# Performance work log

Hardware: AMD Instinct MI355X
Metric: run time of the kernel (lower is better)

## Reference

```python
import jax, jax.numpy as jnp
import numpy as np

NEG_SLOPE = 0.2
EPS = 1e-6


def setup_inputs() -> dict:
    key = jax.random.key(0)
    k1, k2 = jax.random.split(key)
    B, C, N = 4, 64, 32768
    x = jax.random.normal(k1, (B, C, 3, N), dtype=jnp.float32)
    # VNLinear weight: nn.Linear(in, out, bias=False).weight -> [out, in]
    W = jax.random.normal(k2, (C, C), dtype=jnp.float32) * (1.0 / np.sqrt(C))
    return {"x": x, "W": W}


def reference(x, W):
    # VNLinear: kron(W, eye(3)) conv2d == per-3-vector channel mix
    # d[b,o,v,n] = sum_i W[o,i] * x[b,i,v,n]
    d = jnp.einsum('oi,bivn->bovn', W, x)
    dotprod = jnp.sum(x * d, axis=2, keepdims=True)      # [B,C,1,N]
    d_norm_sq = jnp.sum(d * d, axis=2, keepdims=True)    # [B,C,1,N]
    neg = x - (1.0 - NEG_SLOPE) * (dotprod / (d_norm_sq + EPS)) * d
    return jnp.where(dotprod >= 0, x, neg)
```

## Files before the change

kernel.cpp:

```cpp
#include <hip/hip_runtime.h>

#define NEG_SLOPE 0.2f
#define EPS 1e-6f


#define C_CH 64
#define V_DIM 3
#define N_FULL 32768
#define NT 32
#define THREADS 256
#define TPB 4

typedef __attribute__((ext_vector_type(8))) short bf16x8;
typedef __attribute__((ext_vector_type(4))) float f32x4;

__device__ __forceinline__ ushort f2bf(float f) {
    union { float f; unsigned u; } v; v.f = f;
    unsigned r = v.u + 0x7FFFu + ((v.u >> 16) & 1u);
    return (ushort)(r >> 16);
}
__device__ __forceinline__ float bf2f(ushort s) {
    union { unsigned u; float f; } v; v.u = ((unsigned)s) << 16; return v.f;
}
__device__ __forceinline__ unsigned f2u(float f) {
    union { float f; unsigned u; } v; v.f = f; return v.u;
}
__device__ __forceinline__ float u2f(unsigned u) {
    union { unsigned u; float f; } v; v.u = u; return v.f;
}

__global__ __launch_bounds__(THREADS, 3)
void vn_dma_pipe(const float* __restrict__ x,
                 const float* __restrict__ Wf,
                 float* __restrict__ out) {
    __shared__ float xs[2][V_DIM * C_CH * NT];

    const int t     = threadIdx.x;
    const int tile0 = blockIdx.x * TPB;
    const int b     = tile0 >> 10;
    const float* xbase = x   + (size_t)b * (C_CH * V_DIM * N_FULL);
    float*       obase = out + (size_t)b * (C_CH * V_DIM * N_FULL);

    const int lane = t & 63;
    const int w    = t >> 6;
    const int wo   = w >> 1;
    const int wn   = w & 1;
    const int l4   = lane & 15;
    const int hi   = lane >> 4;

    const int slot_r[6] = { (t + 0*THREADS) >> 3, (t + 1*THREADS) >> 3,
                            (t + 2*THREADS) >> 3, (t + 3*THREADS) >> 3,
                            (t + 4*THREADS) >> 3, (t + 5*THREADS) >> 3 };

    bf16x8 Ah[2][2], Al[2][2];
    #pragma unroll
    for (int m = 0; m < 2; ++m)
        #pragma unroll
        for (int kh = 0; kh < 2; ++kh) {
            const float* wp = Wf + (size_t)(wo * 32 + m * 16 + l4) * C_CH + kh * 32 + hi * 8;
            float4 wa = *(const float4*)wp;
            float4 wb = *(const float4*)(wp + 4);
            float wf[8] = {wa.x, wa.y, wa.z, wa.w, wb.x, wb.y, wb.z, wb.w};
            bf16x8 h, l;
            #pragma unroll
            for (int j = 0; j < 8; ++j) {
                ushort hb = f2bf(wf[j]);
                h[j] = (short)hb;
                l[j] = (short)f2bf(wf[j] - bf2f(hb));
            }
            Ah[m][kh] = h; Al[m][kh] = l;
        }

    bf16x8 Aid0, Aid1;
    {
        const int j1 = l4 & 7;
        const bool h0 = (hi == (l4 >> 3));
        const bool h1 = (hi == 2 + (l4 >> 3));
        #pragma unroll
        for (int j = 0; j < 8; ++j) {
            Aid0[j] = (short)((h0 && j == j1) ? 0x3F80 : 0);
            Aid1[j] = (short)((h1 && j == j1) ? 0x3F80 : 0);
        }
    }

    auto stage = [&](int tile, int bf) {
        const float* xb = xbase + ((tile & 1023) << 5);
        #pragma unroll
        for (int it = 0; it < 6; ++it) {
            int slot = t + it * THREADS;
            int r    = slot_r[it];
            int c    = slot & 7;
            int i    = (r * 171) >> 9;
            int cs   = c ^ (((i >> 3) & 1) << 2);
            const float* g = xb + (size_t)r * N_FULL + (cs << 2);
            void* l = (char*)&xs[bf][0] + (size_t)slot * 16;
            __builtin_amdgcn_global_load_lds(
                (const __attribute__((address_space(1))) unsigned*)g,
                (__attribute__((address_space(3))) unsigned*)l, 16, 0, 0);
        }
    };

    stage(tile0, 0);
    __syncthreads();

    const int acol = (wn * 16 + l4) ^ ((hi & 1) << 4);
    const int n    = wn * 16 + l4;

    #pragma unroll
    for (int tt = 0; tt < TPB; ++tt) {
        const int cur = tt & 1;
        const int n0c = ((tile0 + tt) & 1023) << 5;

        if (tt + 1 < TPB) stage(tile0 + tt + 1, cur ^ 1);

        f32x4 acc[2][3], accx[2][3];
        #pragma unroll
        for (int m = 0; m < 2; ++m)
            #pragma unroll
            for (int v = 0; v < 3; ++v) {
                acc[m][v]  = (f32x4){0.f, 0.f, 0.f, 0.f};
                accx[m][v] = (f32x4){0.f, 0.f, 0.f, 0.f};
            }

        #pragma unroll
        for (int v = 0; v < 3; ++v) {
            #pragma unroll
            for (int kh = 0; kh < 2; ++kh) {
                const int ib = kh * 32 + hi * 8;
                float f[8];
                #pragma unroll
                for (int j = 0; j < 8; ++j)
                    f[j] = xs[cur][(3 * (ib + j) + v) * NT + acol];
                union { bf16x8 v8; unsigned d[4]; } BH, BL;
                unsigned rl[8];
                #pragma unroll
                for (int j = 0; j < 8; ++j)
                    rl[j] = f2u(f[j] - u2f(f2u(f[j]) & 0xffff0000u));
                #pragma unroll
                for (int q = 0; q < 4; ++q) {
                    BH.d[q] = __builtin_amdgcn_perm(f2u(f[2 * q + 1]), f2u(f[2 * q]), 0x07060302u);
                    BL.d[q] = __builtin_amdgcn_perm(rl[2 * q + 1], rl[2 * q], 0x07060302u);
                }
                #pragma unroll
                for (int m = 0; m < 2; ++m) {
                    acc[m][v] = __builtin_amdgcn_mfma_f32_16x16x32_bf16(Ah[m][kh], BH.v8, acc[m][v], 0, 0, 0);
                    acc[m][v] = __builtin_amdgcn_mfma_f32_16x16x32_bf16(Ah[m][kh], BL.v8, acc[m][v], 0, 0, 0);
                    acc[m][v] = __builtin_amdgcn_mfma_f32_16x16x32_bf16(Al[m][kh], BH.v8, acc[m][v], 0, 0, 0);
                }
                if (kh == wo) {
                    accx[0][v] = __builtin_amdgcn_mfma_f32_16x16x32_bf16(Aid0, BH.v8, accx[0][v], 0, 0, 0);
                    accx[0][v] = __builtin_amdgcn_mfma_f32_16x16x32_bf16(Aid0, BL.v8, accx[0][v], 0, 0, 0);
                    accx[1][v] = __builtin_amdgcn_mfma_f32_16x16x32_bf16(Aid1, BH.v8, accx[1][v], 0, 0, 0);
                    accx[1][v] = __builtin_amdgcn_mfma_f32_16x16x32_bf16(Aid1, BL.v8, accx[1][v], 0, 0, 0);
                }
            }
        }

        float* ob = obase + n0c + n;
        #pragma unroll
        for (int m = 0; m < 2; ++m) {
            #pragma unroll
            for (int rr = 0; rr < 4; ++rr) {
                const int o = wo * 32 + m * 16 + hi * 4 + rr;
                float xv[3], dv[3];
                #pragma unroll
                for (int v = 0; v < 3; ++v) {
                    xv[v] = accx[m][v][rr];
                    dv[v] = acc[m][v][rr];
                }
                float dot  = xv[0] * dv[0] + xv[1] * dv[1] + xv[2] * dv[2];
                float dnsq = dv[0] * dv[0] + dv[1] * dv[1] + dv[2] * dv[2];
                float f = (1.0f - NEG_SLOPE) * dot * __builtin_amdgcn_rcpf(dnsq + EPS);
                f = (dot >= 0.f) ? 0.f : f;
                float o0 = fmaf(-f, dv[0], xv[0]);
                float o1 = fmaf(-f, dv[1], xv[1]);
                float o2 = fmaf(-f, dv[2], xv[2]);
                float* op = ob + (size_t)o * (V_DIM * N_FULL);
                op[0 * N_FULL] = o0;
                op[1 * N_FULL] = o1;
                op[2 * N_FULL] = o2;
            }
        }

        __syncthreads();
    }
}

extern "C" void kernel_launch(void* const* d_in, const int* in_sizes, int n_in,
                              void* d_out, int out_size, void* d_ws, size_t ws_size,
                              hipStream_t stream) {
    const float* x = (const float*)d_in[0];
    const float* W = (const float*)d_in[1];
    float* out = (float*)d_out;

    const int B = 4;
    const int blocks = B * (N_FULL / NT) / TPB;
    vn_dma_pipe<<<blocks, THREADS, 0, stream>>>(x, W, out);
}
```

Before: 39.93 us.

## Pre-pack x into bf16 hi/lo pairs in LDS via register-staged loads

The async global-to-LDS DMA staging is replaced with register loads of x. Each channel pair is split into packed bf16 hi/lo words once at LDS write time, and the tiles are stored in separate hi and lo arrays with a new swizzle. The MFMA loop then reads four packed dwords per operand instead of eight floats, and does no per-use splitting. This removes redundant conversion work and LDS reads per wave. In exchange it adds register pressure and loses the asynchronous DMA overlap, and the pack/write step now runs after the epilogue.

```diff
diff --git a/kernel.cpp b/kernel.cpp
--- a/kernel.cpp
+++ b/kernel.cpp
@@ -29,11 +29,25 @@
     union { unsigned u; float f; } v; v.u = u; return v.f;
 }
 
+__device__ __forceinline__ void pack_pair(float a, float b,
+                                          unsigned& h, unsigned& l) {
+    unsigned au = f2u(a), bu = f2u(b);
+    unsigned Ar = au + 0x7FFFu + ((au >> 16) & 1u);
+    unsigned Br = bu + 0x7FFFu + ((bu >> 16) & 1u);
+    h = __builtin_amdgcn_perm(Br, Ar, 0x07060302u);
+    unsigned la = f2u(a - u2f(Ar & 0xffff0000u));
+    unsigned lb = f2u(b - u2f(Br & 0xffff0000u));
+    l = __builtin_amdgcn_perm(lb, la, 0x07060302u);
+}
+
+__device__ __forceinline__ int swz(int row) { return ((row >> 2) & 3) << 2; }
+
 __global__ __launch_bounds__(THREADS, 3)
-void vn_dma_pipe(const float* __restrict__ x,
-                 const float* __restrict__ Wf,
-                 float* __restrict__ out) {
-    __shared__ float xs[2][V_DIM * C_CH * NT];
+void vn_pair_pipe(const float* __restrict__ x,
+                  const float* __restrict__ Wf,
+                  float* __restrict__ out) {
+    __shared__ unsigned xh[2][96 * NT];
+    __shared__ unsigned xl[2][96 * NT];
 
     const int t     = threadIdx.x;
     const int tile0 = blockIdx.x * TPB;
@@ -48,9 +62,22 @@
     const int l4   = lane & 15;
     const int hi   = lane >> 4;
 
-    const int slot_r[6] = { (t + 0*THREADS) >> 3, (t + 1*THREADS) >> 3,
-                            (t + 2*THREADS) >> 3, (t + 3*THREADS) >> 3,
-                            (t + 4*THREADS) >> 3, (t + 5*THREADS) >> 3 };
+
+    float4 xa[3], xbv[3];
+    {
+        const float* xg = xbase + ((tile0 & 1023) << 5);
+        #pragma unroll
+        for (int it = 0; it < 3; ++it) {
+            int slot = t + it * THREADS;
+            int row  = slot >> 3;
+            int c4   = (slot & 7) << 2;
+            int v    = row >> 5;
+            int i2   = row & 31;
+            const float* p0 = xg + (size_t)(6 * i2 + v) * N_FULL + c4;
+            xa[it]  = *(const float4*)p0;
+            xbv[it] = *(const float4*)(p0 + 3 * N_FULL);
+        }
+    }
 
     bf16x8 Ah[2][2], Al[2][2];
     #pragma unroll
@@ -83,35 +110,49 @@
         }
     }
 
-    auto stage = [&](int tile, int bf) {
-        const float* xb = xbase + ((tile & 1023) << 5);
-        #pragma unroll
-        for (int it = 0; it < 6; ++it) {
+    auto pack_write = [&](int bf) {
+        #pragma unroll
+        for (int it = 0; it < 3; ++it) {
             int slot = t + it * THREADS;
-            int r    = slot_r[it];
-            int c    = slot & 7;
-            int i    = (r * 171) >> 9;
-            int cs   = c ^ (((i >> 3) & 1) << 2);
-            const float* g = xb + (size_t)r * N_FULL + (cs << 2);
-            void* l = (char*)&xs[bf][0] + (size_t)slot * 16;
-            __builtin_amdgcn_global_load_lds(
-                (const __attribute__((address_space(1))) unsigned*)g,
-                (__attribute__((address_space(3))) unsigned*)l, 16, 0, 0);
+            int row  = slot >> 3;
+            int c4   = (slot & 7) << 2;
+            float a4[4] = {xa[it].x, xa[it].y, xa[it].z, xa[it].w};
+            float b4[4] = {xbv[it].x, xbv[it].y, xbv[it].z, xbv[it].w};
+            unsigned ph[4], pl[4];
+            #pragma unroll
+            for (int q = 0; q < 4; ++q)
+                pack_pair(a4[q], b4[q], ph[q], pl[q]);
+            int col = c4 ^ swz(row);
+            *(uint4*)&xh[bf][row * NT + col] = *(const uint4*)ph;
+            *(uint4*)&xl[bf][row * NT + col] = *(const uint4*)pl;
         }
     };
 
-    stage(tile0, 0);
+    pack_write(0);
     __syncthreads();
 
-    const int acol = (wn * 16 + l4) ^ ((hi & 1) << 4);
-    const int n    = wn * 16 + l4;
+    const int acol2 = (wn * 16 + l4) ^ (hi << 2);
+    const int n     = wn * 16 + l4;
 
     #pragma unroll
     for (int tt = 0; tt < TPB; ++tt) {
         const int cur = tt & 1;
         const int n0c = ((tile0 + tt) & 1023) << 5;
 
-        if (tt + 1 < TPB) stage(tile0 + tt + 1, cur ^ 1);
+        if (tt + 1 < TPB) {
+            const float* xg = xbase + (((tile0 + tt + 1) & 1023) << 5);
+            #pragma unroll
+            for (int it = 0; it < 3; ++it) {
+                int slot = t + it * THREADS;
+                int row  = slot >> 3;
+                int c4   = (slot & 7) << 2;
+                int v    = row >> 5;
+                int i2   = row & 31;
+                const float* p0 = xg + (size_t)(6 * i2 + v) * N_FULL + c4;
+                xa[it]  = *(const float4*)p0;
+                xbv[it] = *(const float4*)(p0 + 3 * N_FULL);
+            }
+        }
 
         f32x4 acc[2][3], accx[2][3];
         #pragma unroll
@@ -126,20 +167,12 @@
         for (int v = 0; v < 3; ++v) {
             #pragma unroll
             for (int kh = 0; kh < 2; ++kh) {
-                const int ib = kh * 32 + hi * 8;
-                float f[8];
-                #pragma unroll
-                for (int j = 0; j < 8; ++j)
-                    f[j] = xs[cur][(3 * (ib + j) + v) * NT + acol];
+                const int rb = v * 32 + kh * 16 + hi * 4;
                 union { bf16x8 v8; unsigned d[4]; } BH, BL;
-                unsigned rl[8];
-                #pragma unroll
-                for (int j = 0; j < 8; ++j)
-                    rl[j] = f2u(f[j] - u2f(f2u(f[j]) & 0xffff0000u));
                 #pragma unroll
                 for (int q = 0; q < 4; ++q) {
-                    BH.d[q] = __builtin_amdgcn_perm(f2u(f[2 * q + 1]), f2u(f[2 * q]), 0x07060302u);
-                    BL.d[q] = __builtin_amdgcn_perm(rl[2 * q + 1], rl[2 * q], 0x07060302u);
+                    BH.d[q] = xh[cur][(rb + q) * NT + acol2];
+                    BL.d[q] = xl[cur][(rb + q) * NT + acol2];
                 }
                 #pragma unroll
                 for (int m = 0; m < 2; ++m) {
@@ -182,6 +215,7 @@
             }
         }
 
+        if (tt + 1 < TPB) pack_write(cur ^ 1);
         __syncthreads();
     }
 }
@@ -195,5 +229,5 @@
 
     const int B = 4;
     const int blocks = B * (N_FULL / NT) / TPB;
-    vn_dma_pipe<<<blocks, THREADS, 0, stream>>>(x, W, out);
-}
+    vn_pair_pipe<<<blocks, THREADS, 0, stream>>>(x, W, out);
+}
```

After: 37.99 us. 1.05x faster.
